# Kernel optimization log

Measured on AMD Instinct MI355X. Metric: run time of the kernel, lower is better.

The kernel has to match this reference:

```python
import jax, jax.numpy as jnp
import numpy as np

W = 4  # kernel_size

def setup_inputs() -> dict:
    key = jax.random.key(0)
    k1, k2, k3, k4 = jax.random.split(key, 4)
    B, T, D, H = 4, 4096, 2048, 256
    x = jax.random.normal(k1, (B, T, D), dtype=jnp.float32)
    # stored as [in, out] (transpose of torch Linear convention)
    w1 = jax.random.normal(k2, (D, H), dtype=jnp.float32) * 0.02
    w2 = jax.random.normal(k3, (H, D * W), dtype=jnp.float32) * 0.02
    b2 = jax.random.normal(k4, (D * W,), dtype=jnp.float32) * 0.02
    return {"x": x, "w1": w1, "w2": w2, "b2": b2}

def reference(x, w1, w2, b2):
    # x: [B, T, D]
    B, T, D = x.shape
    # kernel generator: Linear -> silu -> Linear(+bias)
    h = jax.nn.silu(jnp.einsum('btd,dh->bth', x, w1))
    flat = jnp.einsum('bth,ho->bto', h, w2) + b2          # [B, T, D*W]
    kernels = flat.reshape(B, T, D, W)                    # per-token depthwise kernels
    # causal depthwise dynamic conv: out[t] = sum_w k[t, :, w] * x[t - (W-1) + w]
    xp = jnp.pad(x, ((0, 0), (W - 1, 0), (0, 0)))         # left-pad time by W-1
    out = jnp.zeros_like(x)
    for w in range(W):  # W is a small static constant (4)
        out = out + kernels[..., w] * xp[:, w:w + T, :]
    return jax.nn.silu(out)
```

## Files before the change

### kernel.cpp

```cpp
#include <hip/hip_runtime.h>

typedef unsigned short u16;
typedef unsigned int   u32;
typedef __attribute__((ext_vector_type(8))) short short8;
typedef __attribute__((ext_vector_type(4))) float floatx4;

#define T_DIM 4096
#define D_DIM 2048
#define H_DIM 256
#define M_DIM 16384
#define NFLAT 8192

__device__ __forceinline__ u16 f2bf(float f) {
  union { float f; u32 u; } c; c.f = f;
  u32 x = c.u;
  x += 0x7FFFu + ((x >> 16) & 1u);
  return (u16)(x >> 16);
}
__device__ __forceinline__ u32 pk2(float a, float b) {
  return (u32)f2bf(a) | ((u32)f2bf(b) << 16);
}

__device__ __forceinline__ void glds16(const void* g, void* l) {
  __builtin_amdgcn_global_load_lds(
      (const __attribute__((address_space(1))) void*)g,
      (__attribute__((address_space(3))) void*)l, 16, 0, 0);
}

__global__ void __launch_bounds__(256) tr_cvt_all(const float* __restrict__ w1,
                                                  u16* __restrict__ w1t,
                                                  const float* __restrict__ w2,
                                                  u16* __restrict__ w2t) {
  __shared__ u16 tile[32][33];
  int bid = blockIdx.x;
  const float* src; u16* dst; int R, C, c0, r0;
  if (bid < 512) {
    src = w1; dst = w1t; R = D_DIM; C = H_DIM;
    c0 = (bid & 7) * 32; r0 = (bid >> 3) * 32;
  } else {
    int b = bid - 512;
    src = w2; dst = w2t; R = H_DIM; C = NFLAT;
    c0 = (b & 255) * 32; r0 = (b >> 8) * 32;
  }
  const int tx = threadIdx.x & 31;
  const int ty = threadIdx.x >> 5;
  #pragma unroll
  for (int i = ty; i < 32; i += 8)
    tile[i][tx] = f2bf(src[(size_t)(r0 + i) * C + (c0 + tx)]);
  __syncthreads();
  #pragma unroll
  for (int i = ty; i < 32; i += 8)
    dst[(size_t)(c0 + i) * R + (r0 + tx)] = tile[tx][i];
}

__global__ void __launch_bounds__(256) gemm1_silu(const float* __restrict__ X,
                                                  const u16* __restrict__ Bt,
                                                  u16* __restrict__ H) {
  __shared__ __align__(16) u16 As[2][64][64];
  __shared__ __align__(16) u16 Bs[2][128][64];
  const int tid  = threadIdx.x;
  const int lane = tid & 63, l15 = lane & 15, quad = lane >> 4;
  const int wv   = tid >> 6, wy = wv >> 1, wx = wv & 1;
  const int m0   = blockIdx.y * 64;
  const int n0   = blockIdx.x * 128;
  const int srow = lane >> 3, sc = lane & 7;

  floatx4 acc[2][4];
  const floatx4 zf = {0.f, 0.f, 0.f, 0.f};
  #pragma unroll
  for (int i = 0; i < 2; ++i)
    #pragma unroll
    for (int j = 0; j < 4; ++j) acc[i][j] = zf;

  float4 fA[2][2];

#define G1_LOADA(KT)                                                          \
  _Pragma("unroll")                                                           \
  for (int i = 0; i < 2; ++i) {                                               \
    int s = i * 256 + tid, row = s >> 3, g = s & 7;                           \
    const float* xs = &X[(size_t)(m0 + row) * D_DIM + (KT) * 64 + g * 8];     \
    fA[i][0] = *(const float4*)xs;                                            \
    fA[i][1] = *(const float4*)(xs + 4);                                      \
  }

#define G1_WRITEA(BUF)                                                        \
  _Pragma("unroll")                                                           \
  for (int i = 0; i < 2; ++i) {                                               \
    int s = i * 256 + tid, row = s >> 3, g = s & 7, c = g ^ (row & 7);        \
    uint4 pk;                                                                 \
    pk.x = pk2(fA[i][0].x, fA[i][0].y);                                       \
    pk.y = pk2(fA[i][0].z, fA[i][0].w);                                       \
    pk.z = pk2(fA[i][1].x, fA[i][1].y);                                       \
    pk.w = pk2(fA[i][1].z, fA[i][1].w);                                       \
    *(uint4*)&As[BUF][row][c * 8] = pk;                                       \
  }

#define G1_STAGEB(KT, BUF)                                                    \
  _Pragma("unroll")                                                           \
  for (int ci = 0; ci < 4; ++ci) {                                            \
    int ch  = ci * 4 + wv;                                                    \
    int row = ch * 8 + srow;                                                  \
    glds16(&Bt[(size_t)(n0 + row) * D_DIM + (KT) * 64 + (sc ^ (row & 7)) * 8],\
           (char*)Bs + (BUF) * 16384 + ch * 1024);                            \
  }

  G1_LOADA(0);
  G1_STAGEB(0, 0);
  G1_WRITEA(0);
  G1_LOADA(1);
  __syncthreads();

  #pragma unroll 2
  for (int t = 0; t < 32; ++t) {
    const int b = t & 1;
    if (t + 1 < 32) {
      G1_WRITEA(b ^ 1);
      G1_STAGEB(t + 1, b ^ 1);
    }
    if (t + 2 < 32) G1_LOADA(t + 2);
    short8 af[2][2], bfr[4][2];
    #pragma unroll
    for (int ks = 0; ks < 2; ++ks) {
      #pragma unroll
      for (int mi = 0; mi < 2; ++mi) {
        int row = wy * 32 + mi * 16 + l15;
        af[mi][ks] = *(const short8*)&As[b][row][((ks * 4 + quad) ^ (row & 7)) * 8];
      }
      #pragma unroll
      for (int ni = 0; ni < 4; ++ni) {
        int row = wx * 64 + ni * 16 + l15;
        bfr[ni][ks] = *(const short8*)&Bs[b][row][((ks * 4 + quad) ^ (row & 7)) * 8];
      }
    }
    #pragma unroll
    for (int ks = 0; ks < 2; ++ks)
      #pragma unroll
      for (int mi = 0; mi < 2; ++mi)
        #pragma unroll
        for (int ni = 0; ni < 4; ++ni)
          acc[mi][ni] = __builtin_amdgcn_mfma_f32_16x16x32_bf16(af[mi][ks], bfr[ni][ks], acc[mi][ni], 0, 0, 0);
    if (t + 1 < 32) __syncthreads();
  }

  #pragma unroll
  for (int mi = 0; mi < 2; ++mi)
    #pragma unroll
    for (int ni = 0; ni < 4; ++ni)
      #pragma unroll
      for (int r = 0; r < 4; ++r) {
        float v = acc[mi][ni][r];
        v = v / (1.f + __expf(-v));
        int row = m0 + wy * 32 + mi * 16 + quad * 4 + r;
        int col = n0 + wx * 64 + ni * 16 + l15;
        H[(size_t)row * H_DIM + col] = f2bf(v);
      }
#undef G1_LOADA
#undef G1_WRITEA
#undef G1_STAGEB
}

__global__ void __launch_bounds__(256) gemm2_conv_silu(const u16* __restrict__ Hin,
                                                       const u16* __restrict__ Bt,
                                                       const float* __restrict__ bias,
                                                       const float* __restrict__ X,
                                                       float* __restrict__ Out) {
  __shared__ __align__(16) u16 As[2][128][64];
  __shared__ __align__(16) u16 Bs[2][64][64];
  const int tid  = threadIdx.x;
  const int lane = tid & 63, l15 = lane & 15, quad = lane >> 4;
  const int wv   = tid >> 6;
  const int m0   = blockIdx.y * 128;
  const int d0   = blockIdx.x * 16;
  const int srow = lane >> 3, sc = lane & 7;

  floatx4 acc[2][4];
  const floatx4 zf = {0.f, 0.f, 0.f, 0.f};
  #pragma unroll
  for (int i = 0; i < 2; ++i)
    #pragma unroll
    for (int j = 0; j < 4; ++j) acc[i][j] = zf;

#define G2_STAGE(KT, BUF)                                                     \
  _Pragma("unroll")                                                           \
  for (int ci = 0; ci < 4; ++ci) {                         \
    int ch  = ci * 4 + wv;                                                    \
    int row = ch * 8 + srow;                                                  \
    int g   = (sc ^ (row & 7)) * 8;                                           \
    glds16(&Hin[(size_t)(m0 + row) * H_DIM + (KT) * 64 + g],                  \
           (char*)As + (BUF) * 16384 + ch * 1024);                            \
  }                                                                           \
  _Pragma("unroll")                                                           \
  for (int ci = 0; ci < 2; ++ci) {                          \
    int ch  = ci * 4 + wv;                                                    \
    int rb  = ch * 8 + srow;                                                  \
    int g   = (sc ^ (rb & 7)) * 8;                                            \
    int fc  = (d0 + (rb & 15)) * 4 + (rb >> 4);                               \
    glds16(&Bt[(size_t)fc * H_DIM + (KT) * 64 + g],                           \
           (char*)Bs + (BUF) * 8192 + ch * 1024);                             \
  }

  G2_STAGE(0, 0);
  __syncthreads();

  #pragma unroll
  for (int t = 0; t < 4; ++t) {
    const int b = t & 1;
    if (t + 1 < 4) G2_STAGE(t + 1, b ^ 1);
    short8 af[2][2], bfr[4][2];
    #pragma unroll
    for (int ks = 0; ks < 2; ++ks) {
      #pragma unroll
      for (int mi = 0; mi < 2; ++mi) {
        int row = wv * 32 + mi * 16 + l15;
        af[mi][ks] = *(const short8*)&As[b][row][((ks * 4 + quad) ^ (row & 7)) * 8];
      }
      #pragma unroll
      for (int ni = 0; ni < 4; ++ni) {
        int rb = ni * 16 + l15;
        bfr[ni][ks] = *(const short8*)&Bs[b][rb][((ks * 4 + quad) ^ (rb & 7)) * 8];
      }
    }
    #pragma unroll
    for (int ks = 0; ks < 2; ++ks)
      #pragma unroll
      for (int mi = 0; mi < 2; ++mi)
        #pragma unroll
        for (int ni = 0; ni < 4; ++ni)
          acc[mi][ni] = __builtin_amdgcn_mfma_f32_16x16x32_bf16(af[mi][ks], bfr[ni][ks], acc[mi][ni], 0, 0, 0);
    if (t + 1 < 4) __syncthreads();
  }
#undef G2_STAGE

  const int d     = d0 + l15;
  const float4 bv = *(const float4*)&bias[(size_t)d * 4];
  const int tbase = m0 & (T_DIM - 1);
  const int bbase = m0 - tbase;
  const float* xcol = &X[(size_t)bbase * D_DIM + d];
  float* ocol       = &Out[(size_t)m0 * D_DIM + d];

  #pragma unroll
  for (int mi = 0; mi < 2; ++mi) {
    int t0 = wv * 32 + mi * 16 + quad * 4;
    int tq = tbase + t0;
    float xv[7];
    #pragma unroll
    for (int j = 0; j < 7; ++j) {
      int tt = tq - 3 + j;
      xv[j] = (tt >= 0) ? xcol[(size_t)tt * D_DIM] : 0.f;
    }
    #pragma unroll
    for (int r = 0; r < 4; ++r) {
      float c0 = acc[mi][0][r] + bv.x;
      float c1 = acc[mi][1][r] + bv.y;
      float c2 = acc[mi][2][r] + bv.z;
      float c3 = acc[mi][3][r] + bv.w;
      float o  = c0 * xv[r] + c1 * xv[r + 1] + c2 * xv[r + 2] + c3 * xv[r + 3];
      float y  = o / (1.f + __expf(-o));
      ocol[(size_t)(t0 + r) * D_DIM] = y;
    }
  }
}

extern "C" void kernel_launch(void* const* d_in, const int* in_sizes, int n_in,
                              void* d_out, int out_size, void* d_ws, size_t ws_size,
                              hipStream_t stream) {
  const float* x  = (const float*)d_in[0];
  const float* w1 = (const float*)d_in[1];
  const float* w2 = (const float*)d_in[2];
  const float* b2 = (const float*)d_in[3];
  float* out = (float*)d_out;

  u16* w1t = (u16*)d_ws;
  u16* w2t = w1t + (size_t)H_DIM * D_DIM;
  u16* h   = w2t + (size_t)NFLAT * H_DIM;

  tr_cvt_all<<<512 + 2048, 256, 0, stream>>>(w1, w1t, w2, w2t);
  gemm1_silu<<<dim3(2, M_DIM / 64), 256, 0, stream>>>(x, w1t, h);
  gemm2_conv_silu<<<dim3(D_DIM / 16, M_DIM / 128), 256, 0, stream>>>(h, w2t, b2, x, out);
}
```

Measured before the change: 373.5 us.

## Load gemm2 A fragments straight to registers and stage full-K B tile once

The second GEMM kernel stops double-buffering 64-wide K tiles of both operands through shared memory. Each wave now loads its A fragments (the H rows) directly from global memory into registers covering the whole K=256, and the block stages the full 64x256 B slice into LDS in one pass behind a single barrier. This removes the per-iteration barriers and the LDS round trip for A. In exchange it uses more registers (16 short8 per lane) and loses the overlap between loads and MFMA that the pipelined loop provided.

```diff
diff --git a/kernel.cpp b/kernel.cpp
--- a/kernel.cpp
+++ b/kernel.cpp
@@ -164,14 +164,33 @@
                                                        const float* __restrict__ bias,
                                                        const float* __restrict__ X,
                                                        float* __restrict__ Out) {
-  __shared__ __align__(16) u16 As[2][128][64];
-  __shared__ __align__(16) u16 Bs[2][64][64];
+  __shared__ __align__(16) u16 Bs[64][256];
   const int tid  = threadIdx.x;
   const int lane = tid & 63, l15 = lane & 15, quad = lane >> 4;
   const int wv   = tid >> 6;
   const int m0   = blockIdx.y * 128;
   const int d0   = blockIdx.x * 16;
-  const int srow = lane >> 3, sc = lane & 7;
+
+  #pragma unroll
+  for (int i = 0; i < 8; ++i) {
+    int ch  = wv * 8 + i;
+    int row = ch * 2 + (lane >> 5);
+    int s   = lane & 31;
+    int g   = s ^ (row & 7);
+    int fc  = (d0 + (row & 15)) * 4 + (row >> 4);
+    glds16(&Bt[(size_t)fc * H_DIM + g * 8], (char*)Bs + ch * 1024);
+  }
+
+  short8 af[2][8];
+  #pragma unroll
+  for (int mi = 0; mi < 2; ++mi) {
+    const u16* arow = &Hin[(size_t)(m0 + wv * 32 + mi * 16 + l15) * H_DIM + quad * 8];
+    #pragma unroll
+    for (int ks = 0; ks < 8; ++ks)
+      af[mi][ks] = *(const short8*)(arow + ks * 32);
+  }
+
+  __syncthreads();
 
   floatx4 acc[2][4];
   const floatx4 zf = {0.f, 0.f, 0.f, 0.f};
@@ -180,56 +199,21 @@
     #pragma unroll
     for (int j = 0; j < 4; ++j) acc[i][j] = zf;
 
-#define G2_STAGE(KT, BUF)                                                     \
-  _Pragma("unroll")                                                           \
-  for (int ci = 0; ci < 4; ++ci) {                         \
-    int ch  = ci * 4 + wv;                                                    \
-    int row = ch * 8 + srow;                                                  \
-    int g   = (sc ^ (row & 7)) * 8;                                           \
-    glds16(&Hin[(size_t)(m0 + row) * H_DIM + (KT) * 64 + g],                  \
-           (char*)As + (BUF) * 16384 + ch * 1024);                            \
-  }                                                                           \
-  _Pragma("unroll")                                                           \
-  for (int ci = 0; ci < 2; ++ci) {                          \
-    int ch  = ci * 4 + wv;                                                    \
-    int rb  = ch * 8 + srow;                                                  \
-    int g   = (sc ^ (rb & 7)) * 8;                                            \
-    int fc  = (d0 + (rb & 15)) * 4 + (rb >> 4);                               \
-    glds16(&Bt[(size_t)fc * H_DIM + (KT) * 64 + g],                           \
-           (char*)Bs + (BUF) * 8192 + ch * 1024);                             \
-  }
-
-  G2_STAGE(0, 0);
-  __syncthreads();
-
-  #pragma unroll
-  for (int t = 0; t < 4; ++t) {
-    const int b = t & 1;
-    if (t + 1 < 4) G2_STAGE(t + 1, b ^ 1);
-    short8 af[2][2], bfr[4][2];
-    #pragma unroll
-    for (int ks = 0; ks < 2; ++ks) {
-      #pragma unroll
-      for (int mi = 0; mi < 2; ++mi) {
-        int row = wv * 32 + mi * 16 + l15;
-        af[mi][ks] = *(const short8*)&As[b][row][((ks * 4 + quad) ^ (row & 7)) * 8];
-      }
-      #pragma unroll
-      for (int ni = 0; ni < 4; ++ni) {
-        int rb = ni * 16 + l15;
-        bfr[ni][ks] = *(const short8*)&Bs[b][rb][((ks * 4 + quad) ^ (rb & 7)) * 8];
-      }
-    }
-    #pragma unroll
-    for (int ks = 0; ks < 2; ++ks)
-      #pragma unroll
-      for (int mi = 0; mi < 2; ++mi)
-        #pragma unroll
-        for (int ni = 0; ni < 4; ++ni)
-          acc[mi][ni] = __builtin_amdgcn_mfma_f32_16x16x32_bf16(af[mi][ks], bfr[ni][ks], acc[mi][ni], 0, 0, 0);
-    if (t + 1 < 4) __syncthreads();
-  }
-#undef G2_STAGE
+  #pragma unroll
+  for (int ks = 0; ks < 8; ++ks) {
+    short8 bfr[4];
+    #pragma unroll
+    for (int ni = 0; ni < 4; ++ni) {
+      int rb = ni * 16 + l15;
+      int c  = (ks * 4 + quad) ^ (rb & 7);
+      bfr[ni] = *(const short8*)((const char*)Bs + rb * 512 + c * 16);
+    }
+    #pragma unroll
+    for (int mi = 0; mi < 2; ++mi)
+      #pragma unroll
+      for (int ni = 0; ni < 4; ++ni)
+        acc[mi][ni] = __builtin_amdgcn_mfma_f32_16x16x32_bf16(af[mi][ks], bfr[ni], acc[mi][ni], 0, 0, 0);
+  }
 
   const int d     = d0 + l15;
   const float4 bv = *(const float4*)&bias[(size_t)d * 4];
```

New measurement: 405.0 us. 8.4% more time.
